# Kernel tuning notes

Hardware: AMD Instinct MI355X
Metric: run time of the kernel (lower is better)

The kernel has to match this reference:

```python
import jax, jax.numpy as jnp
import numpy as np

EMBED_DIM = 1024
NUM_HEADS = 16
HEAD_DIM = 64
B, S = 4, 2048


def setup_inputs() -> dict:
    key = jax.random.key(0)
    ks = jax.random.split(key, 5)
    std = 0.02
    x = jax.random.normal(ks[0], (B, S, EMBED_DIM), dtype=jnp.float32)
    Wq = std * jax.random.normal(ks[1], (NUM_HEADS, EMBED_DIM, HEAD_DIM), dtype=jnp.float32)
    Wk = std * jax.random.normal(ks[2], (NUM_HEADS, EMBED_DIM, HEAD_DIM), dtype=jnp.float32)
    Wv = std * jax.random.normal(ks[3], (NUM_HEADS, EMBED_DIM, HEAD_DIM), dtype=jnp.float32)
    Wo = std * jax.random.normal(ks[4], (NUM_HEADS, HEAD_DIM, EMBED_DIM), dtype=jnp.float32)
    bq = jnp.zeros((NUM_HEADS, HEAD_DIM), dtype=jnp.float32)
    bk = jnp.zeros((NUM_HEADS, HEAD_DIM), dtype=jnp.float32)
    bv = jnp.zeros((NUM_HEADS, HEAD_DIM), dtype=jnp.float32)
    bo = jnp.zeros((EMBED_DIM,), dtype=jnp.float32)
    return {"x": x, "Wq": Wq, "bq": bq, "Wk": Wk, "bk": bk,
            "Wv": Wv, "bv": bv, "Wo": Wo, "bo": bo}


def reference(x, Wq, bq, Wk, bk, Wv, bv, Wo, bo):
    # q,k,v: [b, s, n, h]
    q = jnp.einsum('bsd,ndh->bsnh', x, Wq) + bq
    k = jnp.einsum('bsd,ndh->bsnh', x, Wk) + bk
    v = jnp.einsum('bsd,ndh->bsnh', x, Wv) + bv
    scale = 1.0 / (HEAD_DIM ** 0.5)
    # non-causal full attention matrix [b, n, s, t]
    attn = jnp.einsum('bsnh,btnh->bnst', q, k) * scale
    attn = jax.nn.softmax(attn, axis=-1)
    after = jnp.einsum('bnst,btnh->bsnh', attn, v)
    out = jnp.einsum('bsnh,nhd->bsd', after, Wo) + bo
    return out
```

## Files before the change

### kernel.cpp

```cpp
#include <hip/hip_runtime.h>

typedef __bf16 bf16;
typedef bf16 bf16x8 __attribute__((ext_vector_type(8)));
typedef bf16 bf16x4 __attribute__((ext_vector_type(4)));
typedef bf16 bf16x2 __attribute__((ext_vector_type(2)));
typedef float f32x4 __attribute__((ext_vector_type(4)));
typedef float f32x16 __attribute__((ext_vector_type(16)));
typedef unsigned int u32;
typedef u32 u32x4 __attribute__((ext_vector_type(4)));
typedef int i32x2 __attribute__((ext_vector_type(2)));

constexpr int Bb = 4, Ss = 2048, Dd = 1024, NH = 16, HD = 64;
constexpr int BS = Bb * Ss;
constexpr float CSC = 0.18033688011112042f;

__device__ __forceinline__ int sw(int row, int col) {
  return (row << 6) + (col ^ ((row & 7) << 3));
}
__device__ __forceinline__ int sw128(int row, int col) {
  return (row << 7) + (col ^ ((row & 7) << 3));
}

__device__ __forceinline__ void g2l16(const bf16* g, bf16* l) {
  __builtin_amdgcn_global_load_lds(
      (const __attribute__((address_space(1))) void*)g,
      (__attribute__((address_space(3))) void*)l, 16, 0, 0);
}

__device__ __forceinline__ u32 pkbf(float a, float b) {
  bf16x2 v = {(bf16)a, (bf16)b};
  return __builtin_bit_cast(u32, v);
}

__global__ void prep(const float* __restrict__ x, bf16* __restrict__ xb,
                     const float* __restrict__ Wq, const float* __restrict__ Wk,
                     const float* __restrict__ Wv, const float* __restrict__ Wo,
                     const float* __restrict__ bq, const float* __restrict__ bk,
                     const float* __restrict__ bv,
                     bf16* __restrict__ WT_all, bf16* __restrict__ WoT,
                     float* __restrict__ bias_all) {
  __shared__ bf16 Ts[64 * 72];
  const int t = threadIdx.x;
  if (blockIdx.y == 0) {
    int o = (blockIdx.x * 256 + t) * 4;
    f32x4 v = *(const f32x4*)&x[o];
    bf16x4 r = {(bf16)v[0], (bf16)v[1], (bf16)v[2], (bf16)v[3]};
    *(bf16x4*)&xb[o] = r;
    return;
  }
  if (blockIdx.x > 1024) return;
  if (blockIdx.x == 1024) {
    for (int j = t; j < 3072; j += 256) {
      int s2 = j >> 10;
      const float* bb = (s2 == 0) ? bq : (s2 == 1) ? bk : bv;
      bias_all[j] = bb[j & 1023] * (s2 == 0 ? CSC : 1.0f);
    }
    return;
  }
  const int sel = blockIdx.x >> 8, bx = blockIdx.x & 255;
  if (sel < 3) {
    const float* W = (sel == 0) ? Wq : (sel == 1) ? Wk : Wv;
    float scale = (sel == 0) ? CSC : 1.0f;
    int head = bx >> 4, dt = bx & 15;
    const float* src = W + head * 65536 + dt * 64 * 64;
#pragma unroll
    for (int i = 0; i < 4; ++i) {
      int idx = i * 256 + t;
      int dr = idx >> 4, hc = (idx & 15) * 4;
      f32x4 v = *(const f32x4*)&src[dr * 64 + hc];
#pragma unroll
      for (int k = 0; k < 4; ++k) Ts[(hc + k) * 72 + dr] = (bf16)(v[k] * scale);
    }
    __syncthreads();
    bf16* dst = WT_all + (size_t)sel * 1048576 + (size_t)(head * 64) * 1024 + dt * 64;
#pragma unroll
    for (int i = 0; i < 2; ++i) {
      int idx = i * 256 + t;
      int hr = idx >> 3, ch = (idx & 7) * 8;
      *(bf16x8*)&dst[(size_t)hr * 1024 + ch] = *(const bf16x8*)&Ts[hr * 72 + ch];
    }
  } else {
    int ct = bx >> 4, dt = bx & 15;
    const float* src = Wo + (size_t)(ct * 64) * 1024 + dt * 64;
#pragma unroll
    for (int i = 0; i < 4; ++i) {
      int idx = i * 256 + t;
      int cr = idx >> 4, dc = (idx & 15) * 4;
      f32x4 v = *(const f32x4*)&src[(size_t)cr * 1024 + dc];
#pragma unroll
      for (int k = 0; k < 4; ++k) Ts[(dc + k) * 72 + cr] = (bf16)v[k];
    }
    __syncthreads();
    bf16* dst = WoT + (size_t)(dt * 64) * 1024 + ct * 64;
#pragma unroll
    for (int i = 0; i < 2; ++i) {
      int idx = i * 256 + t;
      int dr = idx >> 3, ch = (idx & 7) * 8;
      *(bf16x8*)&dst[(size_t)dr * 1024 + ch] = *(const bf16x8*)&Ts[dr * 72 + ch];
    }
  }
}

__device__ __forceinline__ void gemm_core(const bf16* __restrict__ A,
                                          const bf16* __restrict__ BT,
                                          int m0, int n0, bf16* As, bf16* Bs,
                                          f32x4 (&acc)[4][4]) {
  const int t = threadIdx.x;
  const int l = t & 63, q = l >> 4, lm = l & 15;
  const int w = t >> 6, wm = w & 1, wn = w >> 1;
  int ro[4], co[4];
#pragma unroll
  for (int i = 0; i < 4; ++i) {
    int o = i * 256 + t;
    ro[i] = o >> 3;
    co[i] = ((o & 7) ^ ((o >> 3) & 7)) << 3;
  }
  const int lbase = (t & 192) * 8;
  for (int k0 = 0; k0 < 1024; k0 += 64) {
    __syncthreads();
#pragma unroll
    for (int i = 0; i < 4; ++i)
      g2l16(&A[(size_t)(m0 + ro[i]) * 1024 + k0 + co[i]], &As[i * 2048 + lbase]);
#pragma unroll
    for (int i = 0; i < 4; ++i)
      g2l16(&BT[(size_t)(n0 + ro[i]) * 1024 + k0 + co[i]], &Bs[i * 2048 + lbase]);
    __syncthreads();
#pragma unroll
    for (int kh = 0; kh < 2; ++kh) {
      bf16x8 a[4], b[4];
#pragma unroll
      for (int i = 0; i < 4; ++i)
        a[i] = *(const bf16x8*)&As[sw(wm * 64 + i * 16 + lm, kh * 32 + q * 8)];
#pragma unroll
      for (int i = 0; i < 4; ++i)
        b[i] = *(const bf16x8*)&Bs[sw(wn * 64 + i * 16 + lm, kh * 32 + q * 8)];
#pragma unroll
      for (int mt = 0; mt < 4; ++mt)
#pragma unroll
        for (int nt = 0; nt < 4; ++nt)
          acc[mt][nt] = __builtin_amdgcn_mfma_f32_16x16x32_bf16(a[mt], b[nt], acc[mt][nt], 0, 0, 0);
    }
  }
}

__global__ __launch_bounds__(512, 2) void gemm_qk8(const bf16* __restrict__ A,
                                                   const bf16* __restrict__ BT,
                                                   const float* __restrict__ bias_all,
                                                   bf16* __restrict__ C) {
  __shared__ __align__(16) bf16 SMEM[65536];
  const int t = threadIdx.x;
  const int l = t & 63, q = l >> 4, lm = l & 15;
  const int w = t >> 6, wm = w & 1, wn = w >> 1;
  const int bid = blockIdx.x;
  const int xcd = bid & 7, cc = bid >> 3;
  const int mt = xcd * 4 + (cc >> 3), nt = cc & 7;
  const int m0 = mt * 256, n0 = nt * 256;
  const bf16* Ag = A + (size_t)m0 * 1024;
  const bf16* Bg = BT + (size_t)n0 * 1024;
  const int sR = t >> 3;
  const int sC = t & 7;
  const int dstb = (t & 448) * 8;

  auto stA = [&](int bufb, int h, int kt) {
#pragma unroll
    for (int i = 0; i < 2; ++i) {
      int Lh = i * 64 + sR;
      int gr = ((Lh >> 6) << 7) + h * 64 + (Lh & 63);
      g2l16(&Ag[(size_t)gr * 1024 + kt * 64 + ((sC ^ (Lh & 7)) << 3)],
            &SMEM[bufb * 32768 + h * 8192 + i * 4096 + dstb]);
    }
  };
  auto stB = [&](int bufb, int h, int kt) {
#pragma unroll
    for (int i = 0; i < 2; ++i) {
      int Lh = i * 64 + sR;
      int gr = ((Lh >> 5) << 6) + h * 32 + (Lh & 31);
      g2l16(&Bg[(size_t)gr * 1024 + kt * 64 + ((sC ^ (Lh & 7)) << 3)],
            &SMEM[bufb * 32768 + 16384 + h * 8192 + i * 4096 + dstb]);
    }
  };
  auto rdA = [&](int base, int mt16, int ks) {
    int L = ((mt16 >> 2) << 7) + wm * 64 + ((mt16 & 3) << 4) + lm;
    return *(const bf16x8*)&SMEM[base + sw(L, ks * 32 + q * 8)];
  };
  auto rdB = [&](int base, int nt16, int ks) {
    int L = ((nt16 >> 1) << 7) + wn * 32 + ((nt16 & 1) << 4) + lm;
    return *(const bf16x8*)&SMEM[base + 16384 + sw(L, ks * 32 + q * 8)];
  };

  stA(0, 0, 0); stA(0, 1, 0); stB(0, 0, 0); stB(0, 1, 0);
  stA(1, 0, 1); stB(1, 0, 1);
  asm volatile("s_waitcnt vmcnt(4)" ::: "memory");
  __builtin_amdgcn_s_barrier();
  __builtin_amdgcn_sched_barrier(0);

  f32x4 acc[8][4] = {};
  int cur = 0;
  for (int kt = 0; kt < 16; ++kt, cur ^= 1) {
    const int base = cur * 32768;
    bf16x8 af[4][2], b0[2][2], b1[2][2];
#pragma unroll
    for (int mi = 0; mi < 4; ++mi)
#pragma unroll
      for (int ks = 0; ks < 2; ++ks) af[mi][ks] = rdA(base, mi, ks);
#pragma unroll
    for (int ni = 0; ni < 2; ++ni)
#pragma unroll
      for (int ks = 0; ks < 2; ++ks) b0[ni][ks] = rdB(base, ni, ks);
    if (kt + 1 < 16) { stA(cur ^ 1, 1, kt + 1); stB(cur ^ 1, 1, kt + 1); }
    __builtin_amdgcn_s_barrier();
    __builtin_amdgcn_s_setprio(1);
#pragma unroll
    for (int mi = 0; mi < 4; ++mi)
#pragma unroll
      for (int ni = 0; ni < 2; ++ni)
#pragma unroll
        for (int ks = 0; ks < 2; ++ks)
          acc[mi][ni] = __builtin_amdgcn_mfma_f32_16x16x32_bf16(af[mi][ks], b0[ni][ks], acc[mi][ni], 0, 0, 0);
    __builtin_amdgcn_s_setprio(0);
    __builtin_amdgcn_sched_barrier(0);
    __builtin_amdgcn_s_barrier();
    __builtin_amdgcn_sched_barrier(0);
#pragma unroll
    for (int ni = 0; ni < 2; ++ni)
#pragma unroll
      for (int ks = 0; ks < 2; ++ks) b1[ni][ks] = rdB(base, 2 + ni, ks);
    __builtin_amdgcn_s_barrier();
    __builtin_amdgcn_s_setprio(1);
#pragma unroll
    for (int mi = 0; mi < 4; ++mi)
#pragma unroll
      for (int ni = 0; ni < 2; ++ni)
#pragma unroll
        for (int ks = 0; ks < 2; ++ks)
          acc[mi][2 + ni] = __builtin_amdgcn_mfma_f32_16x16x32_bf16(af[mi][ks], b1[ni][ks], acc[mi][2 + ni], 0, 0, 0);
    __builtin_amdgcn_s_setprio(0);
    __builtin_amdgcn_sched_barrier(0);
    __builtin_amdgcn_s_barrier();
    __builtin_amdgcn_sched_barrier(0);
#pragma unroll
    for (int mi = 0; mi < 4; ++mi)
#pragma unroll
      for (int ks = 0; ks < 2; ++ks) af[mi][ks] = rdA(base, 4 + mi, ks);
#pragma unroll
    for (int ni = 0; ni < 2; ++ni)
#pragma unroll
      for (int ks = 0; ks < 2; ++ks) b0[ni][ks] = rdB(base, ni, ks);
    if (kt + 2 < 16) stA(cur, 0, kt + 2);
    __builtin_amdgcn_s_barrier();
    __builtin_amdgcn_s_setprio(1);
#pragma unroll
    for (int mi = 0; mi < 4; ++mi)
#pragma unroll
      for (int ni = 0; ni < 2; ++ni)
#pragma unroll
        for (int ks = 0; ks < 2; ++ks)
          acc[4 + mi][ni] = __builtin_amdgcn_mfma_f32_16x16x32_bf16(af[mi][ks], b0[ni][ks], acc[4 + mi][ni], 0, 0, 0);
    __builtin_amdgcn_s_setprio(0);
    __builtin_amdgcn_sched_barrier(0);
    __builtin_amdgcn_s_barrier();
    __builtin_amdgcn_sched_barrier(0);
#pragma unroll
    for (int ni = 0; ni < 2; ++ni)
#pragma unroll
      for (int ks = 0; ks < 2; ++ks) b1[ni][ks] = rdB(base, 2 + ni, ks);
    if (kt + 2 < 16) stB(cur, 0, kt + 2);
    __builtin_amdgcn_s_barrier();
    __builtin_amdgcn_s_setprio(1);
#pragma unroll
    for (int mi = 0; mi < 4; ++mi)
#pragma unroll
      for (int ni = 0; ni < 2; ++ni)
#pragma unroll
        for (int ks = 0; ks < 2; ++ks)
          acc[4 + mi][2 + ni] = __builtin_amdgcn_mfma_f32_16x16x32_bf16(af[mi][ks], b1[ni][ks], acc[4 + mi][2 + ni], 0, 0, 0);
    __builtin_amdgcn_s_setprio(0);
    asm volatile("s_waitcnt vmcnt(4)" ::: "memory");
    __builtin_amdgcn_sched_barrier(0);
    __builtin_amdgcn_s_barrier();
    __builtin_amdgcn_sched_barrier(0);
  }
#pragma unroll
  for (int mi = 0; mi < 8; ++mi) {
    int row = m0 + wm * 128 + mi * 16 + q * 4;
#pragma unroll
    for (int ni = 0; ni < 4; ++ni) {
      int col = n0 + wn * 64 + ni * 16 + lm;
      float bb = bias_all[col];
#pragma unroll
      for (int r = 0; r < 4; ++r)
        C[(size_t)(row + r) * 2048 + col] = (bf16)(acc[mi][ni][r] + bb);
    }
  }
}

__global__ __launch_bounds__(256) void gemm_v(const bf16* __restrict__ xb,
                                              const bf16* __restrict__ WT,
                                              const float* __restrict__ bias_all,
                                              bf16* __restrict__ VTb) {
  __shared__ __align__(16) bf16 SMEM[2 * 128 * 64];
  bf16* As = SMEM;
  bf16* Bs = SMEM + 128 * 64;
  const int bid = blockIdx.x;
  const int t = threadIdx.x;
  const int l = t & 63, q = l >> 4, lm = l & 15;
  const int w = t >> 6, wm = w & 1, wn = w >> 1;
  const int xcd = bid & 7, idx = bid >> 3;
  const int m0 = (idx >> 3) * 128;
  const int n0 = (xcd * 8 + (idx & 7)) * 128;
  const bf16* A = WT + (size_t)2048 * 1024;
  const bf16* BT = xb;
  f32x4 acc[4][4] = {};
  gemm_core(A, BT, m0, n0, As, Bs, acc);
  __syncthreads();
#pragma unroll
  for (int nt = 0; nt < 4; ++nt) {
    int sl = wn * 64 + nt * 16 + lm;
#pragma unroll
    for (int mt = 0; mt < 4; ++mt) {
      int ml = wm * 64 + mt * 16 + q * 4;
#pragma unroll
      for (int r = 0; r < 4; ++r)
        SMEM[sw128(ml + r, sl)] = (bf16)(acc[mt][nt][r] + bias_all[2048 + m0 + ml + r]);
    }
  }
  __syncthreads();
  int hh = t >> 1, half = (t & 1) * 64;
  int m = m0 + hh;
  size_t gb = (size_t)((n0 >> 11) * 16 + (m >> 6)) * 131072 +
              (size_t)(m & 63) * 2048 + (n0 & 2047) + half;
#pragma unroll
  for (int k = 0; k < 8; ++k)
    *(bf16x8*)&VTb[gb + k * 8] = *(const bf16x8*)&SMEM[sw128(hh, half + k * 8)];
}

__global__ __launch_bounds__(256) void gemm_out(const bf16* __restrict__ after,
                                                const bf16* __restrict__ WoT,
                                                const float* __restrict__ bo,
                                                float* __restrict__ out) {
  __shared__ __align__(16) bf16 SMEM[2 * 128 * 64];
  const int bid = blockIdx.x;
  const int t = threadIdx.x;
  const int l = t & 63, q = l >> 4, lm = l & 15;
  const int w = t >> 6, wm = w & 1, wn = w >> 1;
  const int xcd = bid & 7, idx = bid >> 3;
  const int n0 = xcd * 128, m0 = idx * 128;
  f32x4 acc[4][4] = {};
  gemm_core(after, WoT, m0, n0, SMEM, SMEM + 128 * 64, acc);
#pragma unroll
  for (int nt = 0; nt < 4; ++nt) {
    int col = n0 + wn * 64 + nt * 16 + lm;
    float bb = bo[col];
#pragma unroll
    for (int mt = 0; mt < 4; ++mt) {
      int row = m0 + wm * 64 + mt * 16 + q * 4;
#pragma unroll
      for (int r = 0; r < 4; ++r)
        out[(size_t)(row + r) * 1024 + col] = acc[mt][nt][r] + bb;
    }
  }
}

__global__ __launch_bounds__(256, 2) void attn(const bf16* __restrict__ QK,
                                               const bf16* __restrict__ VT,
                                               bf16* __restrict__ after) {
  __shared__ __align__(16) bf16 SMEM[32768];
  const int t = threadIdx.x;
  const int l = t & 63, w = t >> 6;
  const int lh = l & 31, H = l >> 5;
  const int f = blockIdx.x;
  const int bn = (f & 7) | ((f >> 6) << 3);
  const int s0 = ((f >> 3) & 7) * 256;
  const int b = bn >> 4, n = bn & 15;
  const bf16* Qb = QK + (size_t)(b * 2048) * 2048 + n * 64;
  const bf16* Kb = Qb + 1024;
  const bf16* Vtb = VT + (size_t)bn * 131072;
  const int rr = t >> 3;
  const int co0 = ((t & 7) ^ (rr & 7)) << 3;
  const int lbase = (t & 192) * 8;
#pragma unroll
  for (int i = 0; i < 8; ++i)
    g2l16(&Qb[(size_t)(s0 + i * 32 + rr) * 2048 + co0], &SMEM[i * 2048 + lbase]);
  __syncthreads();
  bf16x8 qb[2][4];
#pragma unroll
  for (int qt = 0; qt < 2; ++qt)
#pragma unroll
    for (int ks = 0; ks < 4; ++ks)
      qb[qt][ks] = *(const bf16x8*)&SMEM[sw(w * 64 + qt * 32 + lh, ks * 16 + H * 8)];
  __syncthreads();
#pragma unroll
  for (int s = 0; s < 3; ++s)
#pragma unroll
    for (int i = 0; i < 2; ++i) {
      g2l16(&Kb[(size_t)(s * 64 + i * 32 + rr) * 2048 + co0],
            &SMEM[s * 4096 + i * 2048 + lbase]);
      g2l16(&Vtb[(size_t)(i * 32 + rr) * 2048 + s * 64 + co0],
            &SMEM[16384 + s * 4096 + i * 2048 + lbase]);
    }
  f32x16 o_acc[2][2] = {};
  float rsA[2] = {0.f, 0.f}, rsB[2] = {0.f, 0.f};
  for (int rd = 0; rd < 32; ++rd) {
    const int cur = rd & 3;
    const bf16* Ks = &SMEM[cur * 4096];
    const bf16* Vs = &SMEM[16384 + cur * 4096];
    if (rd < 30)       asm volatile("s_waitcnt vmcnt(8)" ::: "memory");
    else if (rd == 30) asm volatile("s_waitcnt vmcnt(4)" ::: "memory");
    else               asm volatile("s_waitcnt vmcnt(0)" ::: "memory");
    __builtin_amdgcn_s_barrier();
    __builtin_amdgcn_sched_barrier(0);
    if (rd <= 28) {
      int st = rd + 3, nb = st & 3, t0n = st * 64;
#pragma unroll
      for (int i = 0; i < 2; ++i) {
        g2l16(&Kb[(size_t)(t0n + i * 32 + rr) * 2048 + co0],
              &SMEM[nb * 4096 + i * 2048 + lbase]);
        g2l16(&Vtb[(size_t)(i * 32 + rr) * 2048 + t0n + co0],
              &SMEM[16384 + nb * 4096 + i * 2048 + lbase]);
      }
    }
#pragma unroll
    for (int tt = 0; tt < 2; ++tt) {
      bf16x8 kb[4];
#pragma unroll
      for (int ks = 0; ks < 4; ++ks)
        kb[ks] = *(const bf16x8*)&Ks[sw(tt * 32 + lh, ks * 16 + H * 8)];
      f32x16 sc[2] = {};
      __builtin_amdgcn_s_setprio(1);
#pragma unroll
      for (int ks = 0; ks < 4; ++ks)
#pragma unroll
        for (int qt = 0; qt < 2; ++qt)
          sc[qt] = __builtin_amdgcn_mfma_f32_32x32x16_bf16(kb[ks], qb[qt][ks], sc[qt], 0, 0, 0);
      __builtin_amdgcn_s_setprio(0);
      u32 pk[2][8];
#pragma unroll
      for (int qt = 0; qt < 2; ++qt)
#pragma unroll
        for (int i = 0; i < 8; ++i) {
          float p0 = __builtin_amdgcn_exp2f(sc[qt][2 * i]);
          float p1 = __builtin_amdgcn_exp2f(sc[qt][2 * i + 1]);
          rsA[qt] += p0;
          rsB[qt] += p1;
          pk[qt][i] = pkbf(p0, p1);
        }
#pragma unroll
      for (int ks2 = 0; ks2 < 2; ++ks2) {
        bf16x8 pa[2];
#pragma unroll
        for (int qt = 0; qt < 2; ++qt) {
          u32x4 av;
#if __has_builtin(__builtin_amdgcn_permlane32_swap)
          i32x2 sA = __builtin_amdgcn_permlane32_swap(
              (int)pk[qt][ks2 * 4 + 0], (int)pk[qt][ks2 * 4 + 2], false, false);
          i32x2 sB = __builtin_amdgcn_permlane32_swap(
              (int)pk[qt][ks2 * 4 + 1], (int)pk[qt][ks2 * 4 + 3], false, false);
          av[0] = (u32)sA[0]; av[1] = (u32)sB[0]; av[2] = (u32)sA[1]; av[3] = (u32)sB[1];
#else
          u32 xx[4];
          xx[0] = __shfl_xor((int)pk[qt][ks2 * 4 + 0], 32);
          xx[1] = __shfl_xor((int)pk[qt][ks2 * 4 + 1], 32);
          xx[2] = __shfl_xor((int)pk[qt][ks2 * 4 + 2], 32);
          xx[3] = __shfl_xor((int)pk[qt][ks2 * 4 + 3], 32);
          av[0] = H ? xx[2] : pk[qt][ks2 * 4 + 0];
          av[1] = H ? xx[3] : pk[qt][ks2 * 4 + 1];
          av[2] = H ? pk[qt][ks2 * 4 + 2] : xx[0];
          av[3] = H ? pk[qt][ks2 * 4 + 3] : xx[1];
#endif
          pa[qt] = __builtin_bit_cast(bf16x8, av);
        }
        __builtin_amdgcn_s_setprio(1);
#pragma unroll
        for (int ht = 0; ht < 2; ++ht) {
          bf16x8 vb = *(const bf16x8*)&Vs[sw(ht * 32 + lh, tt * 32 + ks2 * 16 + H * 8)];
#pragma unroll
          for (int qt = 0; qt < 2; ++qt)
            o_acc[qt][ht] = __builtin_amdgcn_mfma_f32_32x32x16_bf16(pa[qt], vb, o_acc[qt][ht], 0, 0, 0);
        }
        __builtin_amdgcn_s_setprio(0);
      }
    }
  }
#pragma unroll
  for (int qt = 0; qt < 2; ++qt) {
    float rs = rsA[qt] + rsB[qt];
    rs += __shfl_xor(rs, 32);
    float inv = 1.f / rs;
#pragma unroll
    for (int r = 0; r < 16; ++r) {
      int sl = (r & 3) + 8 * (r >> 2) + 4 * H;
      float invr = __shfl(inv, sl);
      size_t base = (size_t)(b * 2048 + s0 + w * 64 + qt * 32 + sl) * 1024 + n * 64;
#pragma unroll
      for (int ht = 0; ht < 2; ++ht)
        after[base + ht * 32 + lh] = (bf16)(o_acc[qt][ht][r] * invr);
    }
  }
}

extern "C" void kernel_launch(void* const* d_in, const int* in_sizes, int n_in,
                              void* d_out, int out_size, void* d_ws, size_t ws_size,
                              hipStream_t stream) {
  const float* x  = (const float*)d_in[0];
  const float* Wq = (const float*)d_in[1];
  const float* bq = (const float*)d_in[2];
  const float* Wk = (const float*)d_in[3];
  const float* bk = (const float*)d_in[4];
  const float* Wv = (const float*)d_in[5];
  const float* bv = (const float*)d_in[6];
  const float* Wo = (const float*)d_in[7];
  const float* bo = (const float*)d_in[8];
  float* out = (float*)d_out;

  bf16* WT_all    = (bf16*)d_ws;
  bf16* WoT       = WT_all + (size_t)3072 * 1024;
  float* bias_all = (float*)(WoT + (size_t)1024 * 1024);
  bf16* xb        = (bf16*)(bias_all + 4096);
  bf16* QKb       = xb + (size_t)BS * Dd;
  bf16* VTb       = QKb + (size_t)BS * 2048;
  bf16* after     = VTb + (size_t)Bb * NH * HD * Ss;

  prep<<<dim3(8192, 2), dim3(256), 0, stream>>>(x, xb, Wq, Wk, Wv, Wo, bq, bk, bv,
                                                WT_all, WoT, bias_all);
  gemm_qk8<<<dim3(256), dim3(512), 0, stream>>>(xb, WT_all, bias_all, QKb);
  gemm_v<<<dim3(512), dim3(256), 0, stream>>>(xb, WT_all, bias_all, VTb);
  attn<<<dim3(512), dim3(256), 0, stream>>>(QKb, VTb, after);
  gemm_out<<<dim3(512), dim3(256), 0, stream>>>(after, WoT, bo, out);
}
```

Before: 264.9 us.

## Replace V and output GEMMs with 8-wave double-buffered pipelined 256x128 kernels

Swaps the simple 128x128 single-buffered gemm_core, which synchronises twice per k-step, for a 512-thread, 256x128-tile core. The new core double-buffers LDS, issues half-tile loads interleaved with MFMA phases, and uses s_setprio and explicit vmcnt waits, in the style of the existing QK kernel. It is used for both the V projection, with a transposed LDS epilogue, and the output projection. It also adds a full vmcnt(0) drain on the penultimate iteration in the QK kernel, apparently a correctness fix for the tail. The larger tiles reduce the block count to 256 with one block per CU, which lowers occupancy.

```diff
diff --git a/kernel.cpp b/kernel.cpp
--- a/kernel.cpp
+++ b/kernel.cpp
@@ -97,48 +97,6 @@
       int idx = i * 256 + t;
       int dr = idx >> 3, ch = (idx & 7) * 8;
       *(bf16x8*)&dst[(size_t)dr * 1024 + ch] = *(const bf16x8*)&Ts[dr * 72 + ch];
-    }
-  }
-}
-
-__device__ __forceinline__ void gemm_core(const bf16* __restrict__ A,
-                                          const bf16* __restrict__ BT,
-                                          int m0, int n0, bf16* As, bf16* Bs,
-                                          f32x4 (&acc)[4][4]) {
-  const int t = threadIdx.x;
-  const int l = t & 63, q = l >> 4, lm = l & 15;
-  const int w = t >> 6, wm = w & 1, wn = w >> 1;
-  int ro[4], co[4];
-#pragma unroll
-  for (int i = 0; i < 4; ++i) {
-    int o = i * 256 + t;
-    ro[i] = o >> 3;
-    co[i] = ((o & 7) ^ ((o >> 3) & 7)) << 3;
-  }
-  const int lbase = (t & 192) * 8;
-  for (int k0 = 0; k0 < 1024; k0 += 64) {
-    __syncthreads();
-#pragma unroll
-    for (int i = 0; i < 4; ++i)
-      g2l16(&A[(size_t)(m0 + ro[i]) * 1024 + k0 + co[i]], &As[i * 2048 + lbase]);
-#pragma unroll
-    for (int i = 0; i < 4; ++i)
-      g2l16(&BT[(size_t)(n0 + ro[i]) * 1024 + k0 + co[i]], &Bs[i * 2048 + lbase]);
-    __syncthreads();
-#pragma unroll
-    for (int kh = 0; kh < 2; ++kh) {
-      bf16x8 a[4], b[4];
-#pragma unroll
-      for (int i = 0; i < 4; ++i)
-        a[i] = *(const bf16x8*)&As[sw(wm * 64 + i * 16 + lm, kh * 32 + q * 8)];
-#pragma unroll
-      for (int i = 0; i < 4; ++i)
-        b[i] = *(const bf16x8*)&Bs[sw(wn * 64 + i * 16 + lm, kh * 32 + q * 8)];
-#pragma unroll
-      for (int mt = 0; mt < 4; ++mt)
-#pragma unroll
-        for (int nt = 0; nt < 4; ++nt)
-          acc[mt][nt] = __builtin_amdgcn_mfma_f32_16x16x32_bf16(a[mt], b[nt], acc[mt][nt], 0, 0, 0);
     }
   }
 }
@@ -275,7 +233,8 @@
         for (int ks = 0; ks < 2; ++ks)
           acc[4 + mi][2 + ni] = __builtin_amdgcn_mfma_f32_16x16x32_bf16(af[mi][ks], b1[ni][ks], acc[4 + mi][2 + ni], 0, 0, 0);
     __builtin_amdgcn_s_setprio(0);
-    asm volatile("s_waitcnt vmcnt(4)" ::: "memory");
+    if (kt == 14) asm volatile("s_waitcnt vmcnt(0)" ::: "memory");
+    else          asm volatile("s_waitcnt vmcnt(4)" ::: "memory");
     __builtin_amdgcn_sched_barrier(0);
     __builtin_amdgcn_s_barrier();
     __builtin_amdgcn_sched_barrier(0);
@@ -294,69 +253,192 @@
   }
 }
 
-__global__ __launch_bounds__(256) void gemm_v(const bf16* __restrict__ xb,
-                                              const bf16* __restrict__ WT,
-                                              const float* __restrict__ bias_all,
-                                              bf16* __restrict__ VTb) {
-  __shared__ __align__(16) bf16 SMEM[2 * 128 * 64];
-  bf16* As = SMEM;
-  bf16* Bs = SMEM + 128 * 64;
-  const int bid = blockIdx.x;
+__device__ __forceinline__ void gemm8_core(const bf16* __restrict__ Ag,
+                                           const bf16* __restrict__ Bg,
+                                           bf16* SMEM, f32x4 (&acc)[4][4]) {
   const int t = threadIdx.x;
   const int l = t & 63, q = l >> 4, lm = l & 15;
-  const int w = t >> 6, wm = w & 1, wn = w >> 1;
-  const int xcd = bid & 7, idx = bid >> 3;
-  const int m0 = (idx >> 3) * 128;
-  const int n0 = (xcd * 8 + (idx & 7)) * 128;
-  const bf16* A = WT + (size_t)2048 * 1024;
-  const bf16* BT = xb;
-  f32x4 acc[4][4] = {};
-  gemm_core(A, BT, m0, n0, As, Bs, acc);
-  __syncthreads();
-#pragma unroll
-  for (int nt = 0; nt < 4; ++nt) {
-    int sl = wn * 64 + nt * 16 + lm;
-#pragma unroll
-    for (int mt = 0; mt < 4; ++mt) {
-      int ml = wm * 64 + mt * 16 + q * 4;
-#pragma unroll
-      for (int r = 0; r < 4; ++r)
-        SMEM[sw128(ml + r, sl)] = (bf16)(acc[mt][nt][r] + bias_all[2048 + m0 + ml + r]);
-    }
-  }
-  __syncthreads();
-  int hh = t >> 1, half = (t & 1) * 64;
-  int m = m0 + hh;
-  size_t gb = (size_t)((n0 >> 11) * 16 + (m >> 6)) * 131072 +
-              (size_t)(m & 63) * 2048 + (n0 & 2047) + half;
-#pragma unroll
-  for (int k = 0; k < 8; ++k)
-    *(bf16x8*)&VTb[gb + k * 8] = *(const bf16x8*)&SMEM[sw128(hh, half + k * 8)];
-}
-
-__global__ __launch_bounds__(256) void gemm_out(const bf16* __restrict__ after,
-                                                const bf16* __restrict__ WoT,
-                                                const float* __restrict__ bo,
-                                                float* __restrict__ out) {
-  __shared__ __align__(16) bf16 SMEM[2 * 128 * 64];
-  const int bid = blockIdx.x;
+  const int w = t >> 6, wm = w >> 1, wn = w & 1;
+  const int sR = t >> 3, sC = t & 7;
+  const int dstb = (t & 448) * 8;
+
+  auto stA = [&](int bufe, int h, int kt) {
+#pragma unroll
+    for (int i = 0; i < 2; ++i) {
+      int Lh = i * 64 + sR;
+      int gr = ((Lh >> 5) << 6) + h * 32 + (Lh & 31);
+      g2l16(&Ag[(size_t)gr * 1024 + kt * 64 + ((sC ^ (Lh & 7)) << 3)],
+            &SMEM[bufe + h * 8192 + i * 4096 + dstb]);
+    }
+  };
+  auto stB = [&](int bufe, int h, int kt) {
+    int gr = ((sR >> 5) << 6) + h * 32 + (sR & 31);
+    g2l16(&Bg[(size_t)gr * 1024 + kt * 64 + ((sC ^ (sR & 7)) << 3)],
+          &SMEM[bufe + 16384 + h * 4096 + dstb]);
+  };
+  auto rdA = [&](int base, int h, int mi, int ks) {
+    int L = wm * 32 + mi * 16 + lm;
+    return *(const bf16x8*)&SMEM[base + h * 8192 + sw(L, ks * 32 + q * 8)];
+  };
+  auto rdB = [&](int base, int h, int ni, int ks) {
+    int L = wn * 32 + ni * 16 + lm;
+    return *(const bf16x8*)&SMEM[base + 16384 + h * 4096 + sw(L, ks * 32 + q * 8)];
+  };
+
+  stA(0, 0, 0); stA(0, 1, 0); stB(0, 0, 0); stB(0, 1, 0);
+  stA(24576, 0, 1); stB(24576, 0, 1);
+  asm volatile("s_waitcnt vmcnt(3)" ::: "memory");
+  __builtin_amdgcn_s_barrier();
+  __builtin_amdgcn_sched_barrier(0);
+
+  int cur = 0;
+  for (int kt = 0; kt < 16; ++kt, cur ^= 1) {
+    const int base = cur * 24576;
+    const int nxt = (cur ^ 1) * 24576;
+    bf16x8 af[2][2], bb[2][2];
+#pragma unroll
+    for (int mi = 0; mi < 2; ++mi)
+#pragma unroll
+      for (int ks = 0; ks < 2; ++ks) af[mi][ks] = rdA(base, 0, mi, ks);
+#pragma unroll
+    for (int ni = 0; ni < 2; ++ni)
+#pragma unroll
+      for (int ks = 0; ks < 2; ++ks) bb[ni][ks] = rdB(base, 0, ni, ks);
+    if (kt + 1 < 16) { stA(nxt, 1, kt + 1); stB(nxt, 1, kt + 1); }
+    __builtin_amdgcn_s_barrier();
+    __builtin_amdgcn_s_setprio(1);
+#pragma unroll
+    for (int mi = 0; mi < 2; ++mi)
+#pragma unroll
+      for (int ni = 0; ni < 2; ++ni)
+#pragma unroll
+        for (int ks = 0; ks < 2; ++ks)
+          acc[mi][ni] = __builtin_amdgcn_mfma_f32_16x16x32_bf16(af[mi][ks], bb[ni][ks], acc[mi][ni], 0, 0, 0);
+    __builtin_amdgcn_s_setprio(0);
+    __builtin_amdgcn_sched_barrier(0);
+    __builtin_amdgcn_s_barrier();
+    __builtin_amdgcn_sched_barrier(0);
+#pragma unroll
+    for (int ni = 0; ni < 2; ++ni)
+#pragma unroll
+      for (int ks = 0; ks < 2; ++ks) bb[ni][ks] = rdB(base, 1, ni, ks);
+    __builtin_amdgcn_s_barrier();
+    __builtin_amdgcn_s_setprio(1);
+#pragma unroll
+    for (int mi = 0; mi < 2; ++mi)
+#pragma unroll
+      for (int ni = 0; ni < 2; ++ni)
+#pragma unroll
+        for (int ks = 0; ks < 2; ++ks)
+          acc[mi][2 + ni] = __builtin_amdgcn_mfma_f32_16x16x32_bf16(af[mi][ks], bb[ni][ks], acc[mi][2 + ni], 0, 0, 0);
+    __builtin_amdgcn_s_setprio(0);
+    __builtin_amdgcn_sched_barrier(0);
+    __builtin_amdgcn_s_barrier();
+    __builtin_amdgcn_sched_barrier(0);
+#pragma unroll
+    for (int mi = 0; mi < 2; ++mi)
+#pragma unroll
+      for (int ks = 0; ks < 2; ++ks) af[mi][ks] = rdA(base, 1, mi, ks);
+#pragma unroll
+    for (int ni = 0; ni < 2; ++ni)
+#pragma unroll
+      for (int ks = 0; ks < 2; ++ks) bb[ni][ks] = rdB(base, 0, ni, ks);
+    if (kt + 2 < 16) stA(base, 0, kt + 2);
+    __builtin_amdgcn_s_barrier();
+    __builtin_amdgcn_s_setprio(1);
+#pragma unroll
+    for (int mi = 0; mi < 2; ++mi)
+#pragma unroll
+      for (int ni = 0; ni < 2; ++ni)
+#pragma unroll
+        for (int ks = 0; ks < 2; ++ks)
+          acc[2 + mi][ni] = __builtin_amdgcn_mfma_f32_16x16x32_bf16(af[mi][ks], bb[ni][ks], acc[2 + mi][ni], 0, 0, 0);
+    __builtin_amdgcn_s_setprio(0);
+    __builtin_amdgcn_sched_barrier(0);
+    __builtin_amdgcn_s_barrier();
+    __builtin_amdgcn_sched_barrier(0);
+#pragma unroll
+    for (int ni = 0; ni < 2; ++ni)
+#pragma unroll
+      for (int ks = 0; ks < 2; ++ks) bb[ni][ks] = rdB(base, 1, ni, ks);
+    if (kt + 2 < 16) stB(base, 0, kt + 2);
+    __builtin_amdgcn_s_barrier();
+    __builtin_amdgcn_s_setprio(1);
+#pragma unroll
+    for (int mi = 0; mi < 2; ++mi)
+#pragma unroll
+      for (int ni = 0; ni < 2; ++ni)
+#pragma unroll
+        for (int ks = 0; ks < 2; ++ks)
+          acc[2 + mi][2 + ni] = __builtin_amdgcn_mfma_f32_16x16x32_bf16(af[mi][ks], bb[ni][ks], acc[2 + mi][2 + ni], 0, 0, 0);
+    __builtin_amdgcn_s_setprio(0);
+    if (kt == 14) asm volatile("s_waitcnt vmcnt(0)" ::: "memory");
+    else          asm volatile("s_waitcnt vmcnt(3)" ::: "memory");
+    __builtin_amdgcn_sched_barrier(0);
+    __builtin_amdgcn_s_barrier();
+    __builtin_amdgcn_sched_barrier(0);
+  }
+}
+
+__global__ __launch_bounds__(512, 1) void gemm8_v(const bf16* __restrict__ xb,
+                                                  const bf16* __restrict__ WvT,
+                                                  const float* __restrict__ bias_all,
+                                                  bf16* __restrict__ VTb) {
+  __shared__ __align__(16) bf16 SMEM[49152];
   const int t = threadIdx.x;
   const int l = t & 63, q = l >> 4, lm = l & 15;
-  const int w = t >> 6, wm = w & 1, wn = w >> 1;
-  const int xcd = bid & 7, idx = bid >> 3;
-  const int n0 = xcd * 128, m0 = idx * 128;
+  const int w = t >> 6, wm = w >> 1, wn = w & 1;
+  const int n0 = (blockIdx.x & 7) * 128;
+  const int m0 = (blockIdx.x >> 3) * 256;
   f32x4 acc[4][4] = {};
-  gemm_core(after, WoT, m0, n0, SMEM, SMEM + 128 * 64, acc);
-#pragma unroll
-  for (int nt = 0; nt < 4; ++nt) {
-    int col = n0 + wn * 64 + nt * 16 + lm;
-    float bb = bo[col];
-#pragma unroll
-    for (int mt = 0; mt < 4; ++mt) {
-      int row = m0 + wm * 64 + mt * 16 + q * 4;
+  gemm8_core(xb + (size_t)m0 * 1024, WvT + (size_t)n0 * 1024, SMEM, acc);
+#pragma unroll
+  for (int a = 0; a < 4; ++a) {
+    int rowL = wm * 64 + a * 16 + q * 4;
+#pragma unroll
+    for (int bi = 0; bi < 4; ++bi) {
+      int colL = wn * 64 + bi * 16 + lm;
+      float bv_ = bias_all[2048 + n0 + colL];
+      int xr = (colL & 7) << 3;
 #pragma unroll
       for (int r = 0; r < 4; ++r)
-        out[(size_t)(row + r) * 1024 + col] = acc[mt][nt][r] + bb;
+        SMEM[(colL << 8) + ((rowL + r) ^ xr)] = (bf16)(acc[a][bi][r] + bv_);
+    }
+  }
+  __syncthreads();
+  const int c = t >> 2, soff = (t & 3) * 64;
+  const int gcol = n0 + c;
+  const int bn = (m0 >> 11) * 16 + (gcol >> 6);
+  const int xr = (c & 7) << 3;
+  size_t gb = (size_t)bn * 131072 + (size_t)(gcol & 63) * 2048 + (m0 & 2047) + soff;
+#pragma unroll
+  for (int k = 0; k < 8; ++k)
+    *(bf16x8*)&VTb[gb + k * 8] =
+        *(const bf16x8*)&SMEM[(c << 8) + soff + ((k * 8) ^ xr)];
+}
+
+__global__ __launch_bounds__(512, 1) void gemm8_out(const bf16* __restrict__ after,
+                                                    const bf16* __restrict__ WoT,
+                                                    const float* __restrict__ bo,
+                                                    float* __restrict__ out) {
+  __shared__ __align__(16) bf16 SMEM[49152];
+  const int t = threadIdx.x;
+  const int l = t & 63, q = l >> 4, lm = l & 15;
+  const int w = t >> 6, wm = w >> 1, wn = w & 1;
+  const int n0 = (blockIdx.x & 7) * 128;
+  const int m0 = (blockIdx.x >> 3) * 256;
+  f32x4 acc[4][4] = {};
+  gemm8_core(after + (size_t)m0 * 1024, WoT + (size_t)n0 * 1024, SMEM, acc);
+#pragma unroll
+  for (int a = 0; a < 4; ++a) {
+    int row = m0 + wm * 64 + a * 16 + q * 4;
+#pragma unroll
+    for (int bi = 0; bi < 4; ++bi) {
+      int col = n0 + wn * 64 + bi * 16 + lm;
+      float bb = bo[col];
+#pragma unroll
+      for (int r = 0; r < 4; ++r)
+        out[(size_t)(row + r) * 1024 + col] = acc[a][bi][r] + bb;
     }
   }
 }
@@ -523,7 +605,8 @@
   prep<<<dim3(8192, 2), dim3(256), 0, stream>>>(x, xb, Wq, Wk, Wv, Wo, bq, bk, bv,
                                                 WT_all, WoT, bias_all);
   gemm_qk8<<<dim3(256), dim3(512), 0, stream>>>(xb, WT_all, bias_all, QKb);
-  gemm_v<<<dim3(512), dim3(256), 0, stream>>>(xb, WT_all, bias_all, VTb);
+  gemm8_v<<<dim3(256), dim3(512), 0, stream>>>(xb, WT_all + (size_t)2048 * 1024,
+                                               bias_all, VTb);
   attn<<<dim3(512), dim3(256), 0, stream>>>(QKb, VTb, after);
-  gemm_out<<<dim3(512), dim3(256), 0, stream>>>(after, WoT, bo, out);
-}
+  gemm8_out<<<dim3(256), dim3(512), 0, stream>>>(after, WoT, bo, out);
+}
```

New measurement: 277.1 us. 1.05x slower.
